# Performance work log

Hardware: AMD Instinct MI355X
Metric: run time of the kernel (lower is better)

## Reference

```python
import jax, jax.numpy as jnp
import numpy as np

B, H, E, K = 8192, 1024, 8, 2


def setup_inputs() -> dict:
    key = jax.random.key(0)
    k1, k2, k3 = jax.random.split(key, 3)
    x = jax.random.normal(k1, (B, H), dtype=jnp.float32)
    gate_w = jax.random.normal(k2, (H, E), dtype=jnp.float32) / np.sqrt(H)
    expert_w = jax.random.normal(k3, (E, H, H), dtype=jnp.float32) / np.sqrt(H)
    return {"x": x, "gate_w": gate_w, "expert_w": expert_w}


def reference(x, gate_w, expert_w):
    # Gate: logits over experts, top-k routing, softmax over the k selected logits
    logits = x @ gate_w                               # [B, E]
    top_w, top_idx = jax.lax.top_k(logits, K)         # [B, K]
    top_w = jax.nn.softmax(top_w, axis=-1)            # softmax over the K selected
    # Combine weights scattered back to [B, E]; zero for unselected experts
    combine = jnp.zeros((x.shape[0], expert_w.shape[0]), dtype=x.dtype)
    combine = combine.at[jnp.arange(x.shape[0])[:, None], top_idx].add(top_w)
    # Expert GEMMs (dense dispatch reference: every expert on every token,
    # masked/weighted by combine; mathematically identical to gather/scatter)
    expert_out = jnp.einsum('bh,eho->beo', x, expert_w)   # [B, E, H]
    out = jnp.einsum('be,beo->bo', combine, expert_out)   # [B, H]
    return out
```

## Files before the change

kernel.cpp:

```cpp
#include <hip/hip_runtime.h>
#include <hip/hip_bf16.h>
#include <stdint.h>

#define B_TOK 8192
#define H_DIM 1024
#define E_NUM 8
#define NSLOT (2 * B_TOK)

typedef __attribute__((ext_vector_type(8))) short short8;
typedef __attribute__((ext_vector_type(4))) float floatx4;

__device__ __forceinline__ unsigned short f32_to_bf16_rne(float f) {
  union { float f; uint32_t u; } v; v.f = f;
  uint32_t u = v.u;
  uint32_t r = u + 0x7FFFu + ((u >> 16) & 1u);
  return (unsigned short)(r >> 16);
}
__device__ __forceinline__ float bf16_to_f32(unsigned short s) {
  union { uint32_t u; float f; } v; v.u = ((uint32_t)s) << 16;
  return v.f;
}

__global__ __launch_bounds__(256) void transpose_w_kernel(const float* __restrict__ w,
                                                          unsigned short* __restrict__ wt) {
  __shared__ float tile[64][68];
  int e = blockIdx.z;
  int k0 = blockIdx.y * 64, n0 = blockIdx.x * 64;
  const float* wb = w + ((size_t)e * H_DIM + k0) * H_DIM + n0;
  unsigned short* wtb = wt + ((size_t)e * H_DIM + n0) * H_DIM + k0;
  int t = threadIdx.x;
  int rr = t >> 4, c4 = t & 15;
#pragma unroll
  for (int j = 0; j < 4; ++j) {
    int r = rr + j * 16;
    float4 v = *(const float4*)(wb + (size_t)r * H_DIM + c4 * 4);
    *(float4*)&tile[r][c4 * 4] = v;
  }
  __syncthreads();
#pragma unroll
  for (int j = 0; j < 4; ++j) {
    int nr = rr + j * 16;
    ushort4 o;
    o.x = f32_to_bf16_rne(tile[c4 * 4 + 0][nr]);
    o.y = f32_to_bf16_rne(tile[c4 * 4 + 1][nr]);
    o.z = f32_to_bf16_rne(tile[c4 * 4 + 2][nr]);
    o.w = f32_to_bf16_rne(tile[c4 * 4 + 3][nr]);
    *(ushort4*)(wtb + (size_t)nr * H_DIM + c4 * 4) = o;
  }
}

__global__ __launch_bounds__(256) void route_kernel(const float* __restrict__ x,
                                                    const float* __restrict__ gw,
                                                    unsigned short* __restrict__ xb,
                                                    int2* __restrict__ re,
                                                    float2* __restrict__ rw) {
  __shared__ float gws[E_NUM][1028];
  int tid = threadIdx.x;
#pragma unroll
  for (int it = 0; it < 8; ++it) {
    int i4 = it * 256 + tid;
    float4 v = ((const float4*)gw)[i4];
    int h = i4 >> 1, e0 = (i4 & 1) * 4;
    gws[e0 + 0][h] = v.x;
    gws[e0 + 1][h] = v.y;
    gws[e0 + 2][h] = v.z;
    gws[e0 + 3][h] = v.w;
  }
  __syncthreads();
  int wid = tid >> 6, lane = tid & 63;
  for (int t = 0; t < 4; ++t) {
    int b = blockIdx.x * 16 + wid * 4 + t;
    const float4* xr = (const float4*)(x + (size_t)b * H_DIM);
    ushort4* xbr = (ushort4*)(xb + (size_t)b * H_DIM);
    float acc[E_NUM];
#pragma unroll
    for (int e = 0; e < E_NUM; e++) acc[e] = 0.f;
#pragma unroll
    for (int it = 0; it < 4; ++it) {
      int c4 = it * 64 + lane;
      float4 v = xr[c4];
      ushort4 o;
      o.x = f32_to_bf16_rne(v.x); o.y = f32_to_bf16_rne(v.y);
      o.z = f32_to_bf16_rne(v.z); o.w = f32_to_bf16_rne(v.w);
      xbr[c4] = o;
      int h = c4 * 4;
#pragma unroll
      for (int e = 0; e < E_NUM; e++) {
        float4 g = *(const float4*)&gws[e][h];
        acc[e] += v.x * g.x + v.y * g.y + v.z * g.z + v.w * g.w;
      }
    }
#pragma unroll
    for (int e = 0; e < E_NUM; e++) {
#pragma unroll
      for (int off = 32; off; off >>= 1) acc[e] += __shfl_xor(acc[e], off, 64);
    }
    if (lane == 0) {
      int e0 = 0; float v0 = acc[0];
#pragma unroll
      for (int e = 1; e < E_NUM; e++) if (acc[e] > v0) { v0 = acc[e]; e0 = e; }
      int e1 = -1; float v1 = -1e30f;
#pragma unroll
      for (int e = 0; e < E_NUM; e++) if (e != e0 && acc[e] > v1) { v1 = acc[e]; e1 = e; }
      float s = expf(v1 - v0);
      float w0 = 1.0f / (1.0f + s);
      re[b] = make_int2(e0, e1);
      rw[b] = make_float2(w0, s * w0);
    }
  }
}

__global__ __launch_bounds__(1024) void compact_kernel(const int2* __restrict__ re,
                                                       int* __restrict__ slot_tok,
                                                       int* __restrict__ yslot,
                                                       int* __restrict__ ebase,
                                                       int* __restrict__ ecnt) {
  __shared__ int wcnt[8][16];
  __shared__ int bless[16];
  int e = blockIdx.x;
  int tid = threadIdx.x, wid = tid >> 6, lane = tid & 63;
  int cless = 0;
  int flag[8];
  unsigned long long mm[8];
#pragma unroll
  for (int it = 0; it < 8; ++it) {
    int2 ee = re[it * 1024 + tid];
    cless += (ee.x < e) + (ee.y < e);
    bool f0 = (ee.x == e), f1 = (ee.y == e);
    flag[it] = f0 ? 1 : (f1 ? 2 : 0);
    mm[it] = __ballot(f0 || f1);
    if (lane == 0) wcnt[it][wid] = __popcll(mm[it]);
  }
#pragma unroll
  for (int off = 32; off; off >>= 1) cless += __shfl_xor(cless, off, 64);
  if (lane == 0) bless[wid] = cless;
  __syncthreads();
  int base = 0;
#pragma unroll
  for (int i = 0; i < 16; ++i) base += bless[i];
  int run = 0;
#pragma unroll
  for (int it = 0; it < 8; ++it) {
    int wbase = 0, total = 0;
#pragma unroll
    for (int i = 0; i < 16; ++i) { int v = wcnt[it][i]; if (i < wid) wbase += v; total += v; }
    if (flag[it]) {
      int pre = __popcll(mm[it] & ((1ull << lane) - 1ull));
      int s = base + run + wbase + pre;
      int t = it * 1024 + tid;
      slot_tok[s] = t;
      yslot[2 * t + (flag[it] == 1 ? 0 : 1)] = s;
    }
    run += total;
  }
  if (tid == 0) { ebase[e] = base; ecnt[e] = run; }
}

__device__ __forceinline__ void async_ld16(const void* g, void* l) {
  __builtin_amdgcn_global_load_lds((const __attribute__((address_space(1))) void*)g,
                                   (__attribute__((address_space(3))) void*)l, 16, 0, 0);
}

__global__ __launch_bounds__(256, 4) void moe_gemm_kernel(
    const unsigned short* __restrict__ xb,
    const unsigned short* __restrict__ wt,
    const int* __restrict__ ebase,
    const int* __restrict__ ecnt,
    const int* __restrict__ slot_tok,
    unsigned short* __restrict__ y) {
  int e = blockIdx.z;
  int c = ecnt[e];
  int m_idx = ((blockIdx.y >> 3) << 3) + blockIdx.x;
  int n_idx = blockIdx.y & 7;
  int m0 = m_idx * 128;
  if (m0 >= c) return;
  int base = ebase[e];
  int n0 = n_idx * 128;

  __shared__ __align__(16) unsigned short As[128 * 32];
  __shared__ __align__(16) unsigned short Bs[128 * 32];

  int tid = threadIdx.x, wid = tid >> 6, lane = tid & 63;
  int rs = wid * 16 + (lane >> 2);
  int swz = (rs >> 1) & 3;
  int kc = ((lane & 3) ^ swz) * 8;
  const int* st = slot_tok + base;
  int ra1 = min(m0 + rs, c - 1);
  int ra2 = min(m0 + 64 + rs, c - 1);
  const unsigned short* gA1 = xb + (size_t)st[ra1] * H_DIM + kc;
  const unsigned short* gA2 = xb + (size_t)st[ra2] * H_DIM + kc;
  const unsigned short* gB1 = wt + ((size_t)e * H_DIM + n0 + rs) * H_DIM + kc;
  const unsigned short* gB2 = wt + ((size_t)e * H_DIM + n0 + 64 + rs) * H_DIM + kc;
  unsigned short* lA1 = As + wid * 512;
  unsigned short* lA2 = As + 2048 + wid * 512;
  unsigned short* lB1 = Bs + wid * 512;
  unsigned short* lB2 = Bs + 2048 + wid * 512;

  floatx4 acc[4][4];
#pragma unroll
  for (int a = 0; a < 4; ++a)
#pragma unroll
    for (int b = 0; b < 4; ++b)
#pragma unroll
      for (int q = 0; q < 4; ++q) acc[a][b][q] = 0.0f;

  int wm = (wid >> 1) * 64, wn = (wid & 1) * 64;
  int mr = lane & 15, kg = lane >> 4;

  for (int ks = 0; ks < H_DIM / 32; ++ks) {
    __syncthreads();
    async_ld16(gA1, lA1);
    async_ld16(gA2, lA2);
    async_ld16(gB1, lB1);
    async_ld16(gB2, lB2);
    gA1 += 32; gA2 += 32; gB1 += 32; gB2 += 32;
    __syncthreads();
    short8 af[4], bfr[4];
#pragma unroll
    for (int t = 0; t < 4; ++t) {
      int rowa = wm + t * 16 + mr;
      int rowb = wn + t * 16 + mr;
      af[t]  = *(const short8*)(const void*)(As + rowa * 32 + ((kg ^ ((rowa >> 1) & 3)) * 8));
      bfr[t] = *(const short8*)(const void*)(Bs + rowb * 32 + ((kg ^ ((rowb >> 1) & 3)) * 8));
    }
#pragma unroll
    for (int tm = 0; tm < 4; ++tm)
#pragma unroll
      for (int tn = 0; tn < 4; ++tn)
        acc[tm][tn] = __builtin_amdgcn_mfma_f32_16x16x32_bf16(af[tm], bfr[tn], acc[tm][tn], 0, 0, 0);
  }

#pragma unroll
  for (int tm = 0; tm < 4; ++tm) {
#pragma unroll
    for (int q = 0; q < 4; ++q) {
      int r = m0 + wm + tm * 16 + kg * 4 + q;
      if (r < c) {
        unsigned short* yrow = y + (size_t)(base + r) * H_DIM + n0 + wn + mr;
#pragma unroll
        for (int tn = 0; tn < 4; ++tn) yrow[tn * 16] = f32_to_bf16_rne(acc[tm][tn][q]);
      }
    }
  }
}

__global__ __launch_bounds__(256) void combine_kernel(const unsigned short* __restrict__ y,
                                                      const int* __restrict__ yslot,
                                                      const float2* __restrict__ rw,
                                                      float* __restrict__ out) {
  int t = blockIdx.x;
  int s0 = yslot[2 * t], s1 = yslot[2 * t + 1];
  float2 w = rw[t];
  const ushort4* y0 = (const ushort4*)(y + (size_t)s0 * H_DIM);
  const ushort4* y1 = (const ushort4*)(y + (size_t)s1 * H_DIM);
  float4* o = (float4*)(out + (size_t)t * H_DIM);
  int i = threadIdx.x;
  ushort4 a = y0[i], b = y1[i];
  float4 r;
  r.x = w.x * bf16_to_f32(a.x) + w.y * bf16_to_f32(b.x);
  r.y = w.x * bf16_to_f32(a.y) + w.y * bf16_to_f32(b.y);
  r.z = w.x * bf16_to_f32(a.z) + w.y * bf16_to_f32(b.z);
  r.w = w.x * bf16_to_f32(a.w) + w.y * bf16_to_f32(b.w);
  o[i] = r;
}

extern "C" void kernel_launch(void* const* d_in, const int* in_sizes, int n_in,
                              void* d_out, int out_size, void* d_ws, size_t ws_size,
                              hipStream_t stream) {
  const float* x  = (const float*)d_in[0];
  const float* gw = (const float*)d_in[1];
  const float* ew = (const float*)d_in[2];
  float* out = (float*)d_out;

  char* ws = (char*)d_ws;
  unsigned short* xb = (unsigned short*)ws;
  unsigned short* wt = (unsigned short*)(ws + (size_t)16 * 1024 * 1024);
  unsigned short* y  = (unsigned short*)(ws + (size_t)32 * 1024 * 1024);
  char* p = ws + (size_t)64 * 1024 * 1024;
  int2*   re       = (int2*)p;
  float2* rw       = (float2*)(p + (64 << 10));
  int*    slot_tok = (int*)(p + (128 << 10));
  int*    yslot    = (int*)(p + (192 << 10));
  int*    ebase    = (int*)(p + (256 << 10));
  int*    ecnt     = (int*)(p + (256 << 10) + 64);

  transpose_w_kernel<<<dim3(16, 16, E_NUM), 256, 0, stream>>>(ew, wt);
  route_kernel<<<512, 256, 0, stream>>>(x, gw, xb, re, rw);
  compact_kernel<<<E_NUM, 1024, 0, stream>>>(re, slot_tok, yslot, ebase, ecnt);
  moe_gemm_kernel<<<dim3(8, 64, E_NUM), 256, 0, stream>>>(
      xb, wt, ebase, ecnt, slot_tok, y);
  combine_kernel<<<B_TOK, 256, 0, stream>>>(y, yslot, rw, out);
}
```

Measured before the change: 182.9 us.

## Fuse transpose and routing kernels, deepen GEMM K-tile, widen combine per block

The weight transpose/bf16 cast and the routing kernel are merged into one prep launch, so both run concurrently in a single grid and one kernel launch is saved. The MoE GEMM K-tile doubles from 32 to 64 with a new 8-way XOR swizzle and more async loads per stage, halving the number of barrier pairs; launch bounds drop to 3 blocks per SM to account for the larger LDS footprint. The combine kernel now processes four tokens per block with one wavefront each. The risks are lower GEMM occupancy and extra LDS pressure, and the transpose tile now uses a 65-float stride with scalar column writes.

```diff
diff --git a/kernel.cpp b/kernel.cpp
--- a/kernel.cpp
+++ b/kernel.cpp
@@ -21,91 +21,96 @@
   return v.f;
 }
 
-__global__ __launch_bounds__(256) void transpose_w_kernel(const float* __restrict__ w,
-                                                          unsigned short* __restrict__ wt) {
-  __shared__ float tile[64][68];
-  int e = blockIdx.z;
-  int k0 = blockIdx.y * 64, n0 = blockIdx.x * 64;
-  const float* wb = w + ((size_t)e * H_DIM + k0) * H_DIM + n0;
-  unsigned short* wtb = wt + ((size_t)e * H_DIM + n0) * H_DIM + k0;
-  int t = threadIdx.x;
-  int rr = t >> 4, c4 = t & 15;
-#pragma unroll
-  for (int j = 0; j < 4; ++j) {
-    int r = rr + j * 16;
-    float4 v = *(const float4*)(wb + (size_t)r * H_DIM + c4 * 4);
-    *(float4*)&tile[r][c4 * 4] = v;
-  }
-  __syncthreads();
-#pragma unroll
-  for (int j = 0; j < 4; ++j) {
-    int nr = rr + j * 16;
-    ushort4 o;
-    o.x = f32_to_bf16_rne(tile[c4 * 4 + 0][nr]);
-    o.y = f32_to_bf16_rne(tile[c4 * 4 + 1][nr]);
-    o.z = f32_to_bf16_rne(tile[c4 * 4 + 2][nr]);
-    o.w = f32_to_bf16_rne(tile[c4 * 4 + 3][nr]);
-    *(ushort4*)(wtb + (size_t)nr * H_DIM + c4 * 4) = o;
-  }
-}
-
-__global__ __launch_bounds__(256) void route_kernel(const float* __restrict__ x,
-                                                    const float* __restrict__ gw,
-                                                    unsigned short* __restrict__ xb,
-                                                    int2* __restrict__ re,
-                                                    float2* __restrict__ rw) {
-  __shared__ float gws[E_NUM][1028];
+__global__ __launch_bounds__(256) void prep_kernel(const float* __restrict__ x,
+                                                   const float* __restrict__ gw,
+                                                   const float* __restrict__ ew,
+                                                   unsigned short* __restrict__ xb,
+                                                   unsigned short* __restrict__ wt,
+                                                   int2* __restrict__ re,
+                                                   float2* __restrict__ rw) {
+  __shared__ float smem[E_NUM * 1028];
+  int bid = blockIdx.x;
   int tid = threadIdx.x;
-#pragma unroll
-  for (int it = 0; it < 8; ++it) {
-    int i4 = it * 256 + tid;
-    float4 v = ((const float4*)gw)[i4];
-    int h = i4 >> 1, e0 = (i4 & 1) * 4;
-    gws[e0 + 0][h] = v.x;
-    gws[e0 + 1][h] = v.y;
-    gws[e0 + 2][h] = v.z;
-    gws[e0 + 3][h] = v.w;
-  }
-  __syncthreads();
-  int wid = tid >> 6, lane = tid & 63;
-  for (int t = 0; t < 4; ++t) {
-    int b = blockIdx.x * 16 + wid * 4 + t;
-    const float4* xr = (const float4*)(x + (size_t)b * H_DIM);
-    ushort4* xbr = (ushort4*)(xb + (size_t)b * H_DIM);
-    float acc[E_NUM];
-#pragma unroll
-    for (int e = 0; e < E_NUM; e++) acc[e] = 0.f;
-#pragma unroll
-    for (int it = 0; it < 4; ++it) {
-      int c4 = it * 64 + lane;
-      float4 v = xr[c4];
+  if (bid < 2048) {
+    float (*tile)[65] = (float(*)[65])smem;
+    int e = bid >> 8;
+    int n0 = ((bid >> 4) & 15) * 64, k0 = (bid & 15) * 64;
+    const float* wb = ew + ((size_t)e * H_DIM + k0) * H_DIM + n0;
+    unsigned short* wtb = wt + ((size_t)e * H_DIM + n0) * H_DIM + k0;
+    int rr = tid >> 4, c4 = tid & 15;
+#pragma unroll
+    for (int j = 0; j < 4; ++j) {
+      int r = rr + j * 16;
+      float4 v = *(const float4*)(wb + (size_t)r * H_DIM + c4 * 4);
+      tile[c4 * 4 + 0][r] = v.x;
+      tile[c4 * 4 + 1][r] = v.y;
+      tile[c4 * 4 + 2][r] = v.z;
+      tile[c4 * 4 + 3][r] = v.w;
+    }
+    __syncthreads();
+#pragma unroll
+    for (int j = 0; j < 4; ++j) {
+      int nr = rr + j * 16;
+      float4 v = *(const float4*)&tile[nr][c4 * 4];
       ushort4 o;
       o.x = f32_to_bf16_rne(v.x); o.y = f32_to_bf16_rne(v.y);
       o.z = f32_to_bf16_rne(v.z); o.w = f32_to_bf16_rne(v.w);
-      xbr[c4] = o;
-      int h = c4 * 4;
+      *(ushort4*)(wtb + (size_t)nr * H_DIM + c4 * 4) = o;
+    }
+  } else {
+    int rb = bid - 2048;
+    float (*gws)[1028] = (float(*)[1028])smem;
+#pragma unroll
+    for (int it = 0; it < 8; ++it) {
+      int i4 = it * 256 + tid;
+      float4 v = ((const float4*)gw)[i4];
+      int h = i4 >> 1, e0 = (i4 & 1) * 4;
+      gws[e0 + 0][h] = v.x;
+      gws[e0 + 1][h] = v.y;
+      gws[e0 + 2][h] = v.z;
+      gws[e0 + 3][h] = v.w;
+    }
+    __syncthreads();
+    int wid = tid >> 6, lane = tid & 63;
+    for (int t = 0; t < 4; ++t) {
+      int b = rb * 16 + wid * 4 + t;
+      const float4* xr = (const float4*)(x + (size_t)b * H_DIM);
+      ushort4* xbr = (ushort4*)(xb + (size_t)b * H_DIM);
+      float acc[E_NUM];
+#pragma unroll
+      for (int e = 0; e < E_NUM; e++) acc[e] = 0.f;
+#pragma unroll
+      for (int it = 0; it < 4; ++it) {
+        int c4 = it * 64 + lane;
+        float4 v = xr[c4];
+        ushort4 o;
+        o.x = f32_to_bf16_rne(v.x); o.y = f32_to_bf16_rne(v.y);
+        o.z = f32_to_bf16_rne(v.z); o.w = f32_to_bf16_rne(v.w);
+        xbr[c4] = o;
+        int h = c4 * 4;
+#pragma unroll
+        for (int e = 0; e < E_NUM; e++) {
+          float4 g = *(const float4*)&gws[e][h];
+          acc[e] += v.x * g.x + v.y * g.y + v.z * g.z + v.w * g.w;
+        }
+      }
 #pragma unroll
       for (int e = 0; e < E_NUM; e++) {
-        float4 g = *(const float4*)&gws[e][h];
-        acc[e] += v.x * g.x + v.y * g.y + v.z * g.z + v.w * g.w;
-      }
-    }
-#pragma unroll
-    for (int e = 0; e < E_NUM; e++) {
-#pragma unroll
-      for (int off = 32; off; off >>= 1) acc[e] += __shfl_xor(acc[e], off, 64);
-    }
-    if (lane == 0) {
-      int e0 = 0; float v0 = acc[0];
-#pragma unroll
-      for (int e = 1; e < E_NUM; e++) if (acc[e] > v0) { v0 = acc[e]; e0 = e; }
-      int e1 = -1; float v1 = -1e30f;
-#pragma unroll
-      for (int e = 0; e < E_NUM; e++) if (e != e0 && acc[e] > v1) { v1 = acc[e]; e1 = e; }
-      float s = expf(v1 - v0);
-      float w0 = 1.0f / (1.0f + s);
-      re[b] = make_int2(e0, e1);
-      rw[b] = make_float2(w0, s * w0);
+#pragma unroll
+        for (int off = 32; off; off >>= 1) acc[e] += __shfl_xor(acc[e], off, 64);
+      }
+      if (lane == 0) {
+        int e0 = 0; float v0 = acc[0];
+#pragma unroll
+        for (int e = 1; e < E_NUM; e++) if (acc[e] > v0) { v0 = acc[e]; e0 = e; }
+        int e1 = -1; float v1 = -1e30f;
+#pragma unroll
+        for (int e = 0; e < E_NUM; e++) if (e != e0 && acc[e] > v1) { v1 = acc[e]; e1 = e; }
+        float s = expf(v1 - v0);
+        float w0 = 1.0f / (1.0f + s);
+        re[b] = make_int2(e0, e1);
+        rw[b] = make_float2(w0, s * w0);
+      }
     }
   }
 }
@@ -161,7 +166,7 @@
                                    (__attribute__((address_space(3))) void*)l, 16, 0, 0);
 }
 
-__global__ __launch_bounds__(256, 4) void moe_gemm_kernel(
+__global__ __launch_bounds__(256, 3) void moe_gemm_kernel(
     const unsigned short* __restrict__ xb,
     const unsigned short* __restrict__ wt,
     const int* __restrict__ ebase,
@@ -177,24 +182,28 @@
   int base = ebase[e];
   int n0 = n_idx * 128;
 
-  __shared__ __align__(16) unsigned short As[128 * 32];
-  __shared__ __align__(16) unsigned short Bs[128 * 32];
+  __shared__ __align__(16) unsigned short As[128 * 64];
+  __shared__ __align__(16) unsigned short Bs[128 * 64];
 
   int tid = threadIdx.x, wid = tid >> 6, lane = tid & 63;
-  int rs = wid * 16 + (lane >> 2);
-  int swz = (rs >> 1) & 3;
-  int kc = ((lane & 3) ^ swz) * 8;
+  int rloc = lane >> 3;
+  int cl = lane & 7;
   const int* st = slot_tok + base;
-  int ra1 = min(m0 + rs, c - 1);
-  int ra2 = min(m0 + 64 + rs, c - 1);
-  const unsigned short* gA1 = xb + (size_t)st[ra1] * H_DIM + kc;
-  const unsigned short* gA2 = xb + (size_t)st[ra2] * H_DIM + kc;
-  const unsigned short* gB1 = wt + ((size_t)e * H_DIM + n0 + rs) * H_DIM + kc;
-  const unsigned short* gB2 = wt + ((size_t)e * H_DIM + n0 + 64 + rs) * H_DIM + kc;
-  unsigned short* lA1 = As + wid * 512;
-  unsigned short* lA2 = As + 2048 + wid * 512;
-  unsigned short* lB1 = Bs + wid * 512;
-  unsigned short* lB2 = Bs + 2048 + wid * 512;
+
+  const unsigned short* gA[4];
+  const unsigned short* gB[4];
+  unsigned short* lA[4];
+  unsigned short* lB[4];
+#pragma unroll
+  for (int j = 0; j < 4; ++j) {
+    int rl = wid * 32 + j * 8 + rloc;
+    int g = (cl ^ (rl & 7)) * 8;
+    int ra = min(m0 + rl, c - 1);
+    gA[j] = xb + (size_t)st[ra] * H_DIM + g;
+    gB[j] = wt + ((size_t)e * H_DIM + n0 + rl) * H_DIM + g;
+    lA[j] = As + (wid * 32 + j * 8) * 64;
+    lB[j] = Bs + (wid * 32 + j * 8) * 64;
+  }
 
   floatx4 acc[4][4];
 #pragma unroll
@@ -206,28 +215,33 @@
 
   int wm = (wid >> 1) * 64, wn = (wid & 1) * 64;
   int mr = lane & 15, kg = lane >> 4;
-
-  for (int ks = 0; ks < H_DIM / 32; ++ks) {
+  int sw = mr & 7;
+
+  for (int ks = 0; ks < 16; ++ks) {
     __syncthreads();
-    async_ld16(gA1, lA1);
-    async_ld16(gA2, lA2);
-    async_ld16(gB1, lB1);
-    async_ld16(gB2, lB2);
-    gA1 += 32; gA2 += 32; gB1 += 32; gB2 += 32;
+#pragma unroll
+    for (int j = 0; j < 4; ++j) {
+      async_ld16(gA[j], lA[j]);
+      async_ld16(gB[j], lB[j]);
+    }
+#pragma unroll
+    for (int j = 0; j < 4; ++j) { gA[j] += 64; gB[j] += 64; }
     __syncthreads();
-    short8 af[4], bfr[4];
-#pragma unroll
-    for (int t = 0; t < 4; ++t) {
-      int rowa = wm + t * 16 + mr;
-      int rowb = wn + t * 16 + mr;
-      af[t]  = *(const short8*)(const void*)(As + rowa * 32 + ((kg ^ ((rowa >> 1) & 3)) * 8));
-      bfr[t] = *(const short8*)(const void*)(Bs + rowb * 32 + ((kg ^ ((rowb >> 1) & 3)) * 8));
-    }
-#pragma unroll
-    for (int tm = 0; tm < 4; ++tm)
-#pragma unroll
-      for (int tn = 0; tn < 4; ++tn)
-        acc[tm][tn] = __builtin_amdgcn_mfma_f32_16x16x32_bf16(af[tm], bfr[tn], acc[tm][tn], 0, 0, 0);
+#pragma unroll
+    for (int kk = 0; kk < 2; ++kk) {
+      int cb = ((kk * 4 + kg) ^ sw) * 8;
+      short8 af[4], bfr[4];
+#pragma unroll
+      for (int t = 0; t < 4; ++t) {
+        af[t]  = *(const short8*)(const void*)(As + (wm + t * 16 + mr) * 64 + cb);
+        bfr[t] = *(const short8*)(const void*)(Bs + (wn + t * 16 + mr) * 64 + cb);
+      }
+#pragma unroll
+      for (int tm = 0; tm < 4; ++tm)
+#pragma unroll
+        for (int tn = 0; tn < 4; ++tn)
+          acc[tm][tn] = __builtin_amdgcn_mfma_f32_16x16x32_bf16(af[tm], bfr[tn], acc[tm][tn], 0, 0, 0);
+    }
   }
 
 #pragma unroll
@@ -248,20 +262,30 @@
                                                       const int* __restrict__ yslot,
                                                       const float2* __restrict__ rw,
                                                       float* __restrict__ out) {
-  int t = blockIdx.x;
+  int wid = threadIdx.x >> 6, lane = threadIdx.x & 63;
+  int t = blockIdx.x * 4 + wid;
   int s0 = yslot[2 * t], s1 = yslot[2 * t + 1];
   float2 w = rw[t];
   const ushort4* y0 = (const ushort4*)(y + (size_t)s0 * H_DIM);
   const ushort4* y1 = (const ushort4*)(y + (size_t)s1 * H_DIM);
   float4* o = (float4*)(out + (size_t)t * H_DIM);
-  int i = threadIdx.x;
-  ushort4 a = y0[i], b = y1[i];
-  float4 r;
-  r.x = w.x * bf16_to_f32(a.x) + w.y * bf16_to_f32(b.x);
-  r.y = w.x * bf16_to_f32(a.y) + w.y * bf16_to_f32(b.y);
-  r.z = w.x * bf16_to_f32(a.z) + w.y * bf16_to_f32(b.z);
-  r.w = w.x * bf16_to_f32(a.w) + w.y * bf16_to_f32(b.w);
-  o[i] = r;
+  ushort4 a[4], b[4];
+#pragma unroll
+  for (int j = 0; j < 4; ++j) {
+    int i = j * 64 + lane;
+    a[j] = y0[i];
+    b[j] = y1[i];
+  }
+#pragma unroll
+  for (int j = 0; j < 4; ++j) {
+    int i = j * 64 + lane;
+    float4 r;
+    r.x = w.x * bf16_to_f32(a[j].x) + w.y * bf16_to_f32(b[j].x);
+    r.y = w.x * bf16_to_f32(a[j].y) + w.y * bf16_to_f32(b[j].y);
+    r.z = w.x * bf16_to_f32(a[j].z) + w.y * bf16_to_f32(b[j].z);
+    r.w = w.x * bf16_to_f32(a[j].w) + w.y * bf16_to_f32(b[j].w);
+    o[i] = r;
+  }
 }
 
 extern "C" void kernel_launch(void* const* d_in, const int* in_sizes, int n_in,
@@ -284,10 +308,9 @@
   int*    ebase    = (int*)(p + (256 << 10));
   int*    ecnt     = (int*)(p + (256 << 10) + 64);
 
-  transpose_w_kernel<<<dim3(16, 16, E_NUM), 256, 0, stream>>>(ew, wt);
-  route_kernel<<<512, 256, 0, stream>>>(x, gw, xb, re, rw);
+  prep_kernel<<<2560, 256, 0, stream>>>(x, gw, ew, xb, wt, re, rw);
   compact_kernel<<<E_NUM, 1024, 0, stream>>>(re, slot_tok, yslot, ebase, ecnt);
   moe_gemm_kernel<<<dim3(8, 64, E_NUM), 256, 0, stream>>>(
       xb, wt, ebase, ecnt, slot_tok, y);
-  combine_kernel<<<B_TOK, 256, 0, stream>>>(y, yslot, rw, out);
-}
+  combine_kernel<<<B_TOK / 4, 256, 0, stream>>>(y, yslot, rw, out);
+}
```

After: 170.5 us. -6.8%, faster.
